# Kernel tuning notes

Measured on AMD Instinct MI355X. Metric: run time of the kernel, lower is better.

Reference implementation:

```python
import jax, jax.numpy as jnp
import numpy as np

B = 2048          # batch_size from init
D = 512           # embedding dim
TAU = 0.5         # temperature
EPS = 1e-12       # torch F.normalize eps


def _l2_normalize(x):
    n = jnp.linalg.norm(x, axis=1, keepdims=True)
    return x / jnp.maximum(n, EPS)


def setup_inputs() -> dict:
    key = jax.random.key(0)
    k1, k2 = jax.random.split(key)
    emb_i = jax.random.normal(k1, (2 * B, D), dtype=jnp.float32)
    emb_j = jax.random.normal(k2, (2 * B, D), dtype=jnp.float32)
    return {"emb_i": emb_i, "emb_j": emb_j}


def reference(emb_i, emb_j):
    z_i = _l2_normalize(emb_i)
    z_j = _l2_normalize(emb_j)
    rep = jnp.concatenate([z_i, z_j], axis=0)        # [4B, D], unit rows
    # cosine similarity of unit vectors == plain GEMM
    sim = rep @ rep.T                                # [4B, 4B]
    n = 4 * B
    pos1 = jnp.concatenate([jnp.diagonal(sim, B), jnp.diagonal(sim, -B)])        # [6B]
    pos2 = jnp.concatenate([jnp.diagonal(sim, 2 * B), jnp.diagonal(sim, -2 * B)])  # [4B]
    pos3 = jnp.concatenate([jnp.diagonal(sim, 3 * B), jnp.diagonal(sim, -3 * B)])  # [2B]
    nominator = (jnp.sum(jnp.exp(pos1 / TAU))
                 + jnp.sum(jnp.exp(pos2 / TAU))
                 + jnp.sum(jnp.exp(pos3 / TAU)))
    off_diag = 1.0 - jnp.eye(n, dtype=sim.dtype)
    denominator = jnp.sum(off_diag * jnp.exp(sim / TAU)) - nominator
    loss = -jnp.log(nominator / denominator) / (4 * B)
    return loss
```

## Files before the change

kernel.cpp:

```cpp
#include <hip/hip_runtime.h>
#include <stdint.h>

#define DIM       512
#define NROWS     8192
#define HALF_ROWS 4096
#define TILE      128
#define BK        32

typedef float  floatx4 __attribute__((ext_vector_type(4)));
typedef __bf16 bf16x8  __attribute__((ext_vector_type(8)));

__device__ __forceinline__ void async_copy16(const unsigned short* g, unsigned short* l) {
    __builtin_amdgcn_global_load_lds(
        (const __attribute__((address_space(1))) uint32_t*)(g),
        (__attribute__((address_space(3))) uint32_t*)(l),
        16, 0, 0);
}

__global__ void init_ws(double* ws) {
    ws[0] = 0.0;
    ws[1] = 0.0;
}

__global__ __launch_bounds__(256) void normalize_kernel(
    const float* __restrict__ emb_i, const float* __restrict__ emb_j,
    unsigned short* __restrict__ rep)
{
    const int wave = threadIdx.x >> 6;
    const int lane = threadIdx.x & 63;
    const int row  = blockIdx.x * 4 + wave;
    const float* src = (row < HALF_ROWS) ? (emb_i + (size_t)row * DIM)
                                         : (emb_j + (size_t)(row - HALF_ROWS) * DIM);
    const int c = lane * 8;
    float4 v0 = *(const float4*)(src + c);
    float4 v1 = *(const float4*)(src + c + 4);
    float s = v0.x*v0.x + v0.y*v0.y + v0.z*v0.z + v0.w*v0.w
            + v1.x*v1.x + v1.y*v1.y + v1.z*v1.z + v1.w*v1.w;
    #pragma unroll
    for (int off = 32; off; off >>= 1) s += __shfl_xor(s, off, 64);
    const float nrm = sqrtf(s);
    const float inv = 1.0f / fmaxf(nrm, 1e-12f);
    float f[8] = {v0.x*inv, v0.y*inv, v0.z*inv, v0.w*inv,
                  v1.x*inv, v1.y*inv, v1.z*inv, v1.w*inv};
    union { unsigned short h[8]; uint4 u; } pk;
    #pragma unroll
    for (int t = 0; t < 8; ++t) {
        uint32_t b = __float_as_uint(f[t]);
        b += 0x7FFFu + ((b >> 16) & 1u);
        pk.h[t] = (unsigned short)(b >> 16);
    }
    *(uint4*)(rep + (size_t)row * DIM + c) = pk.u;
}

__global__ __launch_bounds__(256) void gram_kernel(
    const unsigned short* __restrict__ rep, double* __restrict__ ws)
{
    const int bj = blockIdx.x, bi = blockIdx.y;
    if (bj < bi) return;

    __shared__ unsigned short As[TILE * BK];
    __shared__ unsigned short Bs[TILE * BK];
    __shared__ float red[8];

    const int tid  = threadIdx.x;
    const int wave = tid >> 6, lane = tid & 63;
    const int wm = wave >> 1, wn = wave & 1;
    const int m = lane & 15, quad = lane >> 4;

    floatx4 acc[4][4];
    #pragma unroll
    for (int a = 0; a < 4; ++a)
        #pragma unroll
        for (int b = 0; b < 4; ++b)
            #pragma unroll
            for (int e = 0; e < 4; ++e) acc[a][b][e] = 0.0f;

    const int i0 = bi * TILE, j0 = bj * TILE;

    for (int k0 = 0; k0 < DIM; k0 += BK) {
        #pragma unroll
        for (int r = 0; r < 2; ++r) {
            const int chunk = r * 256 + tid;
            const int row   = chunk >> 2;
            const int cc    = (chunk & 3) * 8;
            async_copy16(rep + (size_t)(i0 + row) * DIM + k0 + cc, As + chunk * 8);
            async_copy16(rep + (size_t)(j0 + row) * DIM + k0 + cc, Bs + chunk * 8);
        }
        __syncthreads();

        bf16x8 af[4], bfr[4];
        #pragma unroll
        for (int mt = 0; mt < 4; ++mt)
            af[mt] = *(const bf16x8*)(As + (wm * 64 + mt * 16 + m) * BK + quad * 8);
        #pragma unroll
        for (int nt = 0; nt < 4; ++nt)
            bfr[nt] = *(const bf16x8*)(Bs + (wn * 64 + nt * 16 + m) * BK + quad * 8);
        #pragma unroll
        for (int mt = 0; mt < 4; ++mt)
            #pragma unroll
            for (int nt = 0; nt < 4; ++nt)
                acc[mt][nt] = __builtin_amdgcn_mfma_f32_16x16x32_bf16(
                    af[mt], bfr[nt], acc[mt][nt], 0, 0, 0);
        __syncthreads();
    }

    float s_all = 0.0f, s_pos = 0.0f;
    const float LOG2E2 = 2.885390081777927f;
    #pragma unroll
    for (int mt = 0; mt < 4; ++mt) {
        const int ibase = i0 + wm * 64 + mt * 16 + quad * 4;
        #pragma unroll
        for (int nt = 0; nt < 4; ++nt) {
            const int j = j0 + wn * 64 + nt * 16 + m;
            const floatx4 a = acc[mt][nt];
            #pragma unroll
            for (int r2 = 0; r2 < 4; ++r2) {
                const int i = ibase + r2;
                const float e = exp2f(a[r2] * LOG2E2);
                if (i != j) s_all += e;
                const int d = j - i;
                if (d == 2048 || d == 4096 || d == 6144) s_pos += e;
            }
        }
    }
    #pragma unroll
    for (int off = 32; off; off >>= 1) {
        s_all += __shfl_xor(s_all, off, 64);
        s_pos += __shfl_xor(s_pos, off, 64);
    }
    if (lane == 0) { red[wave] = s_all; red[4 + wave] = s_pos; }
    __syncthreads();
    if (tid == 0) {
        const float w  = (bi == bj) ? 1.0f : 2.0f;
        const float ta = (red[0] + red[1] + red[2] + red[3]) * w;
        const float tp = (red[4] + red[5] + red[6] + red[7]) * w;
        atomicAdd(&ws[0], (double)ta);
        atomicAdd(&ws[1], (double)tp);
    }
}

__global__ void finalize_kernel(const double* __restrict__ ws, float* __restrict__ out) {
    const double nom = ws[1];
    const double den = ws[0] - nom;
    out[0] = (float)(-log(nom / den) / (double)NROWS);
}

extern "C" void kernel_launch(void* const* d_in, const int* in_sizes, int n_in,
                              void* d_out, int out_size, void* d_ws, size_t ws_size,
                              hipStream_t stream) {
    const float* emb_i = (const float*)d_in[0];
    const float* emb_j = (const float*)d_in[1];
    float* out = (float*)d_out;
    double* ws = (double*)d_ws;
    unsigned short* rep = (unsigned short*)((char*)d_ws + 256);

    hipLaunchKernelGGL(init_ws, dim3(1), dim3(1), 0, stream, ws);
    hipLaunchKernelGGL(normalize_kernel, dim3(NROWS / 4), dim3(256), 0, stream,
                       emb_i, emb_j, rep);
    hipLaunchKernelGGL(gram_kernel, dim3(64, 64), dim3(256), 0, stream, rep, ws);
    hipLaunchKernelGGL(finalize_kernel, dim3(1), dim3(1), 0, stream, ws, out);
}
```

Before: 147.8 us.

## Double-buffer gram kernel, swizzle LDS, compact triangular grid, fuse init and finalize

Restructures the Gram kernel with BK=64 double-buffered LDS staging, where the next K tile is loaded while MFMAs run on the current one, and adds an XOR swizzle to avoid LDS bank conflicts. The 64x64 grid, half of whose blocks exited early, becomes a 1D grid of only the 2080 upper-triangle tiles, mapped with an XCD-aware index and a sqrt-based triangular decode. The init and finalize kernels are folded into the normalize kernel and into a last-block-done atomic counter, cutting two launches. Risks include the float sqrt tile mapping needing correction loops, and a plain barrier with vmcnt waits instead of __syncthreads.

```diff
diff --git a/kernel.cpp b/kernel.cpp
--- a/kernel.cpp
+++ b/kernel.cpp
@@ -1,11 +1,15 @@
 #include <hip/hip_runtime.h>
 #include <stdint.h>
+#include <math.h>
 
 #define DIM       512
 #define NROWS     8192
 #define HALF_ROWS 4096
 #define TILE      128
-#define BK        32
+#define BK        64
+#define NT        64
+#define NTRI      2080
+#define CPX       260
 
 typedef float  floatx4 __attribute__((ext_vector_type(4)));
 typedef __bf16 bf16x8  __attribute__((ext_vector_type(8)));
@@ -17,15 +21,14 @@
         16, 0, 0);
 }
 
-__global__ void init_ws(double* ws) {
-    ws[0] = 0.0;
-    ws[1] = 0.0;
-}
-
 __global__ __launch_bounds__(256) void normalize_kernel(
     const float* __restrict__ emb_i, const float* __restrict__ emb_j,
-    unsigned short* __restrict__ rep)
+    unsigned short* __restrict__ rep, double* __restrict__ ws)
 {
+    if (blockIdx.x == 0 && threadIdx.x == 0) {
+        ws[0] = 0.0; ws[1] = 0.0;
+        ((unsigned long long*)ws)[2] = 0ull;
+    }
     const int wave = threadIdx.x >> 6;
     const int lane = threadIdx.x & 63;
     const int row  = blockIdx.x * 4 + wave;
@@ -38,8 +41,7 @@
             + v1.x*v1.x + v1.y*v1.y + v1.z*v1.z + v1.w*v1.w;
     #pragma unroll
     for (int off = 32; off; off >>= 1) s += __shfl_xor(s, off, 64);
-    const float nrm = sqrtf(s);
-    const float inv = 1.0f / fmaxf(nrm, 1e-12f);
+    const float inv = 1.0f / fmaxf(sqrtf(s), 1e-12f);
     float f[8] = {v0.x*inv, v0.y*inv, v0.z*inv, v0.w*inv,
                   v1.x*inv, v1.y*inv, v1.z*inv, v1.w*inv};
     union { unsigned short h[8]; uint4 u; } pk;
@@ -52,20 +54,71 @@
     *(uint4*)(rep + (size_t)row * DIM + c) = pk.u;
 }
 
+__device__ __forceinline__ void stage_tile(const unsigned short* __restrict__ rep,
+    int i0, int j0, int k0, unsigned short* A, unsigned short* Bb, int tid)
+{
+    #pragma unroll
+    for (int l = 0; l < 4; ++l) {
+        const int ch  = l * 256 + tid;
+        const int row = ch >> 3;
+        const int s   = ch & 7;
+        const int col = (s ^ (row & 7)) << 3;
+        async_copy16(rep + (size_t)(i0 + row) * DIM + k0 + col, A  + ch * 8);
+        async_copy16(rep + (size_t)(j0 + row) * DIM + k0 + col, Bb + ch * 8);
+    }
+}
+
+#define WAIT_VM0() asm volatile("s_waitcnt vmcnt(0)" ::: "memory")
+
+#define COMPUTE_TILE(CUR) do { \
+    bf16x8 af[4][2], bf[4][2]; \
+    _Pragma("unroll") \
+    for (int mt = 0; mt < 4; ++mt) { \
+        const char* rp = (const char*)(sA[CUR]) + (size_t)(wm * 64 + mt * 16 + m) * 128; \
+        af[mt][0] = *(const bf16x8*)(rp + ((quad * 16) ^ swz)); \
+        af[mt][1] = *(const bf16x8*)(rp + ((64 + quad * 16) ^ swz)); \
+    } \
+    _Pragma("unroll") \
+    for (int nt = 0; nt < 4; ++nt) { \
+        const char* rp = (const char*)(sB[CUR]) + (size_t)(wn * 64 + nt * 16 + m) * 128; \
+        bf[nt][0] = *(const bf16x8*)(rp + ((quad * 16) ^ swz)); \
+        bf[nt][1] = *(const bf16x8*)(rp + ((64 + quad * 16) ^ swz)); \
+    } \
+    asm volatile("s_waitcnt lgkmcnt(0)" ::: "memory"); \
+    __builtin_amdgcn_sched_barrier(0); \
+    __builtin_amdgcn_s_setprio(1); \
+    _Pragma("unroll") \
+    for (int mt = 0; mt < 4; ++mt) \
+        _Pragma("unroll") \
+        for (int nt = 0; nt < 4; ++nt) \
+            _Pragma("unroll") \
+            for (int ks = 0; ks < 2; ++ks) \
+                acc[mt][nt] = __builtin_amdgcn_mfma_f32_16x16x32_bf16( \
+                    af[mt][ks], bf[nt][ks], acc[mt][nt], 0, 0, 0); \
+    __builtin_amdgcn_s_setprio(0); \
+} while (0)
+
 __global__ __launch_bounds__(256) void gram_kernel(
-    const unsigned short* __restrict__ rep, double* __restrict__ ws)
+    const unsigned short* __restrict__ rep, double* __restrict__ ws,
+    float* __restrict__ out)
 {
-    const int bj = blockIdx.x, bi = blockIdx.y;
-    if (bj < bi) return;
-
-    __shared__ unsigned short As[TILE * BK];
-    __shared__ unsigned short Bs[TILE * BK];
+    __shared__ unsigned short sA[2][TILE * BK];
+    __shared__ unsigned short sB[2][TILE * BK];
     __shared__ float red[8];
 
     const int tid  = threadIdx.x;
     const int wave = tid >> 6, lane = tid & 63;
     const int wm = wave >> 1, wn = wave & 1;
     const int m = lane & 15, quad = lane >> 4;
+    const int swz = (m & 7) << 4;
+
+    const int u = (blockIdx.x & 7) * CPX + (blockIdx.x >> 3);
+    int bi = (int)((2.0f * NT + 1.0f
+             - sqrtf((2.0f * NT + 1.0f) * (2.0f * NT + 1.0f) - 8.0f * (float)u)) * 0.5f);
+    while ((bi + 1) * NT - ((bi + 1) * bi) / 2 <= u) ++bi;
+    while (bi * NT - (bi * (bi - 1)) / 2 > u) --bi;
+    const int bj = bi + (u - (bi * NT - (bi * (bi - 1)) / 2));
+    const int i0 = bi * TILE, j0 = bj * TILE;
 
     floatx4 acc[4][4];
     #pragma unroll
@@ -75,34 +128,21 @@
             #pragma unroll
             for (int e = 0; e < 4; ++e) acc[a][b][e] = 0.0f;
 
-    const int i0 = bi * TILE, j0 = bj * TILE;
-
-    for (int k0 = 0; k0 < DIM; k0 += BK) {
-        #pragma unroll
-        for (int r = 0; r < 2; ++r) {
-            const int chunk = r * 256 + tid;
-            const int row   = chunk >> 2;
-            const int cc    = (chunk & 3) * 8;
-            async_copy16(rep + (size_t)(i0 + row) * DIM + k0 + cc, As + chunk * 8);
-            async_copy16(rep + (size_t)(j0 + row) * DIM + k0 + cc, Bs + chunk * 8);
-        }
-        __syncthreads();
-
-        bf16x8 af[4], bfr[4];
-        #pragma unroll
-        for (int mt = 0; mt < 4; ++mt)
-            af[mt] = *(const bf16x8*)(As + (wm * 64 + mt * 16 + m) * BK + quad * 8);
-        #pragma unroll
-        for (int nt = 0; nt < 4; ++nt)
-            bfr[nt] = *(const bf16x8*)(Bs + (wn * 64 + nt * 16 + m) * BK + quad * 8);
-        #pragma unroll
-        for (int mt = 0; mt < 4; ++mt)
-            #pragma unroll
-            for (int nt = 0; nt < 4; ++nt)
-                acc[mt][nt] = __builtin_amdgcn_mfma_f32_16x16x32_bf16(
-                    af[mt], bfr[nt], acc[mt][nt], 0, 0, 0);
-        __syncthreads();
-    }
+    stage_tile(rep, i0, j0, 0, sA[0], sB[0], tid);
+    WAIT_VM0();
+    __builtin_amdgcn_s_barrier();
+    __builtin_amdgcn_sched_barrier(0);
+
+    int cur = 0;
+    for (int t = 0; t < 7; ++t) {
+        stage_tile(rep, i0, j0, (t + 1) * BK, sA[cur ^ 1], sB[cur ^ 1], tid);
+        COMPUTE_TILE(cur);
+        WAIT_VM0();
+        __builtin_amdgcn_s_barrier();
+        __builtin_amdgcn_sched_barrier(0);
+        cur ^= 1;
+    }
+    COMPUTE_TILE(cur);
 
     float s_all = 0.0f, s_pos = 0.0f;
     const float LOG2E2 = 2.885390081777927f;
@@ -112,14 +152,14 @@
         #pragma unroll
         for (int nt = 0; nt < 4; ++nt) {
             const int j = j0 + wn * 64 + nt * 16 + m;
-            const floatx4 a = acc[mt][nt];
+            const floatx4 v = acc[mt][nt];
             #pragma unroll
             for (int r2 = 0; r2 < 4; ++r2) {
                 const int i = ibase + r2;
-                const float e = exp2f(a[r2] * LOG2E2);
-                if (i != j) s_all += e;
+                const float ex = exp2f(v[r2] * LOG2E2);
+                if (i != j) s_all += ex;
                 const int d = j - i;
-                if (d == 2048 || d == 4096 || d == 6144) s_pos += e;
+                if (d == 2048 || d == 4096 || d == 6144) s_pos += ex;
             }
         }
     }
@@ -131,18 +171,21 @@
     if (lane == 0) { red[wave] = s_all; red[4 + wave] = s_pos; }
     __syncthreads();
     if (tid == 0) {
-        const float w  = (bi == bj) ? 1.0f : 2.0f;
-        const float ta = (red[0] + red[1] + red[2] + red[3]) * w;
-        const float tp = (red[4] + red[5] + red[6] + red[7]) * w;
+        const float wgt = (bi == bj) ? 1.0f : 2.0f;
+        const float ta = (red[0] + red[1] + red[2] + red[3]) * wgt;
+        const float tp = (red[4] + red[5] + red[6] + red[7]) * wgt;
         atomicAdd(&ws[0], (double)ta);
         atomicAdd(&ws[1], (double)tp);
-    }
-}
-
-__global__ void finalize_kernel(const double* __restrict__ ws, float* __restrict__ out) {
-    const double nom = ws[1];
-    const double den = ws[0] - nom;
-    out[0] = (float)(-log(nom / den) / (double)NROWS);
+        __threadfence();
+        unsigned* ctr = (unsigned*)(ws + 2);
+        const unsigned done = atomicAdd(ctr, 1u);
+        if (done == NTRI - 1) {
+            __threadfence();
+            const double nom = atomicAdd(&ws[1], 0.0);
+            const double den = atomicAdd(&ws[0], 0.0) - nom;
+            out[0] = (float)(-log(nom / den) / (double)NROWS);
+        }
+    }
 }
 
 extern "C" void kernel_launch(void* const* d_in, const int* in_sizes, int n_in,
@@ -154,9 +197,7 @@
     double* ws = (double*)d_ws;
     unsigned short* rep = (unsigned short*)((char*)d_ws + 256);
 
-    hipLaunchKernelGGL(init_ws, dim3(1), dim3(1), 0, stream, ws);
     hipLaunchKernelGGL(normalize_kernel, dim3(NROWS / 4), dim3(256), 0, stream,
-                       emb_i, emb_j, rep);
-    hipLaunchKernelGGL(gram_kernel, dim3(64, 64), dim3(256), 0, stream, rep, ws);
-    hipLaunchKernelGGL(finalize_kernel, dim3(1), dim3(1), 0, stream, ws, out);
-}
+                       emb_i, emb_j, rep, ws);
+    hipLaunchKernelGGL(gram_kernel, dim3(NTRI), dim3(256), 0, stream, rep, ws, out);
+}
```

After: 173.8 us. 1.18x slower.
